# Kernel tuning notes

Measured on AMD Instinct MI355X. Metric: run time of the kernel, lower is better.

Reference implementation:

```python
import jax, jax.numpy as jnp
import numpy as np

T, D, E, F, K = 2048, 1024, 16, 512, 2  # tokens, hidden, experts, expert d_ff, top_k
NORM_TOPK = True


def setup_inputs() -> dict:
    key = jax.random.key(0)
    k0, k1, k2, k3 = jax.random.split(key, 4)
    hidden_states = jax.random.normal(k0, (T, D), jnp.float32)
    w_gate = jax.random.normal(k1, (E, D), jnp.float32) * (D ** -0.5)      # router Linear(D, E), no bias
    w13 = jax.random.normal(k2, (E, 2 * F, D), jnp.float32) * (D ** -0.5)  # fused gate+up proj per expert
    w2 = jax.random.normal(k3, (E, D, F), jnp.float32) * (F ** -0.5)       # down proj per expert
    return {"hidden_states": hidden_states, "w_gate": w_gate, "w13": w13, "w2": w2}


def reference(hidden_states, w_gate, w13, w2):
    # Router: softmax (fp32) -> top-k -> optional renorm
    logits = hidden_states @ w_gate.T                                   # [T, E]
    probs = jax.nn.softmax(logits.astype(jnp.float32), axis=-1)
    weights, selected = jax.lax.top_k(probs, K)                          # [T, K]
    if NORM_TOPK:
        weights = weights / jnp.sum(weights, axis=-1, keepdims=True)
    weights = weights.astype(hidden_states.dtype)

    # Sparse combine matrix: combine[t, e] = routing weight iff expert e selected for token t
    combine = jnp.zeros((T, E), hidden_states.dtype)
    combine = combine.at[jnp.arange(T)[:, None], selected].add(weights)

    # Expert FFN (computed for all experts, zeroed by combine; faithful math)
    h = jnp.einsum('td,efd->tef', hidden_states, w13)                    # [T, E, 2F]
    gate, up = jnp.split(h, 2, axis=-1)
    act = jax.nn.silu(gate) * up                                         # SiluAndMul, [T, E, F]
    y = jnp.einsum('tef,edf->ted', act, w2)                              # [T, E, D]
    return jnp.einsum('ted,te->td', y, combine)                          # [T, D]
```

## Files before the change

kernel.cpp:

```cpp
#include <hip/hip_runtime.h>
#include <hip/hip_bf16.h>
#include <math.h>

#define T_TOK 2048
#define DIM   1024
#define NEXP  16
#define FDIM  512
#define TOPK  2

#define BM 128
#define BN 64
#define BK 32

typedef float f32x4 __attribute__((ext_vector_type(4)));
typedef short s16x8 __attribute__((ext_vector_type(8)));

static __device__ __forceinline__ ushort f2bf(float f) {
  union { float f; unsigned u; } v; v.f = f;
  unsigned u = v.u;
  unsigned r = u + 0x7fffu + ((u >> 16) & 1u);
  return (ushort)(r >> 16);
}
static __device__ __forceinline__ float bf2f(ushort h) {
  union { unsigned u; float f; } v; v.u = ((unsigned)h) << 16; return v.f;
}
static __device__ __forceinline__ void split2(float f, ushort& h, ushort& l) {
  ushort hb = f2bf(f);
  h = hb;
  l = f2bf(f - bf2f(hb));
}

__global__ __launch_bounds__(64) void router_k(const float* __restrict__ x,
                                               const float* __restrict__ wg,
                                               int* __restrict__ sel,
                                               float* __restrict__ wt,
                                               int* __restrict__ cnt) {
  int t = blockIdx.x;
  int lane = threadIdx.x;
  const float* xr = x + (size_t)t * DIM;
  float acc[NEXP];
#pragma unroll
  for (int e = 0; e < NEXP; ++e) acc[e] = 0.f;
  for (int d0 = 0; d0 < DIM; d0 += 64) {
    float xv = xr[d0 + lane];
#pragma unroll
    for (int e = 0; e < NEXP; ++e) acc[e] += xv * wg[e * DIM + d0 + lane];
  }
#pragma unroll
  for (int e = 0; e < NEXP; ++e) {
    float v = acc[e];
    v += __shfl_xor(v, 32); v += __shfl_xor(v, 16); v += __shfl_xor(v, 8);
    v += __shfl_xor(v, 4);  v += __shfl_xor(v, 2);  v += __shfl_xor(v, 1);
    acc[e] = v;
  }
  if (lane == 0) {
    float b1 = -1e30f, b2 = -1e30f; int i1 = 0, i2 = 0;
#pragma unroll
    for (int e = 0; e < NEXP; ++e) {
      float v = acc[e];
      if (v > b1) { b2 = b1; i2 = i1; b1 = v; i1 = e; }
      else if (v > b2) { b2 = v; i2 = e; }
    }
    float r = expf(b2 - b1);
    float w2v = r / (1.f + r);
    float w1v = 1.f - w2v;
    sel[t * 2 + 0] = i1; sel[t * 2 + 1] = i2;
    wt[t * 2 + 0] = w1v; wt[t * 2 + 1] = w2v;
    atomicAdd(&cnt[i1], 1);
    atomicAdd(&cnt[i2], 1);
  }
}

__global__ __launch_bounds__(256) void xsplit_k(const float* __restrict__ x,
                                                ushort* __restrict__ xhi,
                                                ushort* __restrict__ xlo) {
  int idx = (blockIdx.x * 256 + threadIdx.x) * 4;
  float4 v = *(const float4*)(x + idx);
  ushort h0,h1,h2,h3,l0,l1,l2,l3;
  split2(v.x, h0, l0); split2(v.y, h1, l1);
  split2(v.z, h2, l2); split2(v.w, h3, l3);
  *(ushort4*)(xhi + idx) = make_ushort4(h0, h1, h2, h3);
  *(ushort4*)(xlo + idx) = make_ushort4(l0, l1, l2, l3);
}

__global__ void offsets_k(const int* __restrict__ cnt, int* __restrict__ off) {
  if (threadIdx.x == 0 && blockIdx.x == 0) {
    int s = 0;
#pragma unroll
    for (int e = 0; e < NEXP; ++e) { off[e] = s; s += cnt[e]; }
    off[NEXP] = s;
  }
}

__global__ __launch_bounds__(256) void fill_k(const int* __restrict__ sel,
                                              const float* __restrict__ wt,
                                              const int* __restrict__ off,
                                              int* __restrict__ cnt2,
                                              int* __restrict__ rowtok,
                                              float* __restrict__ rowwt) {
  int i = blockIdx.x * 256 + threadIdx.x;
  if (i >= T_TOK * TOPK) return;
  int e = sel[i];
  int pos = off[e] + atomicAdd(&cnt2[e], 1);
  rowtok[pos] = i >> 1;
  rowwt[pos] = wt[i];
}

__global__ __launch_bounds__(256, 2) void gemm1_k(const ushort* __restrict__ xhi,
                                                  const ushort* __restrict__ xlo,
                                                  const float* __restrict__ w13,
                                                  const int* __restrict__ off,
                                                  const int* __restrict__ rowtok,
                                                  float* __restrict__ H) {
  int e = blockIdx.z;
  int rbeg = off[e];
  int rows = off[e + 1] - rbeg;
  int m0 = blockIdx.y * BM;
  if (m0 >= rows) return;
  int n0 = blockIdx.x * BN;

  __shared__ ushort Ah[BM * BK], Al[BM * BK], Bh[BN * BK], Bl[BN * BK];
  __shared__ int toksh[BM];

  int tid = threadIdx.x;
  if (tid < BM) {
    int r = m0 + tid;
    toksh[tid] = rowtok[rbeg + (r < rows ? r : rows - 1)];
  }
  __syncthreads();

  int srow = tid >> 2;
  int sc = tid & 3;
  int tok0 = toksh[srow];
  int tok1 = toksh[srow + 64];
  const ushort* a0h = xhi + (size_t)tok0 * DIM + sc * 8;
  const ushort* a0l = xlo + (size_t)tok0 * DIM + sc * 8;
  const ushort* a1h = xhi + (size_t)tok1 * DIM + sc * 8;
  const ushort* a1l = xlo + (size_t)tok1 * DIM + sc * 8;
  const float*  bsrc = w13 + ((size_t)e * (2 * FDIM) + (n0 + srow)) * DIM + sc * 8;

  int boA0 = (srow * 64 + sc * 16) ^ ((srow & 7) << 4);
  int boA1 = ((srow + 64) * 64 + sc * 16) ^ ((srow & 7) << 4);
  int boB  = boA0;

  f32x4 acc[4][2];
#pragma unroll
  for (int a = 0; a < 4; ++a)
#pragma unroll
    for (int b = 0; b < 2; ++b) acc[a][b] = {0.f, 0.f, 0.f, 0.f};

  int lane = tid & 63;
  int w = tid >> 6;
  int wm = (w & 1) * 64, wn = (w >> 1) * 32;
  int lr = lane & 15, lk = lane >> 4;

  uint4 rA0h, rA0l, rA1h, rA1l;
  float4 rB0, rB1;

  rA0h = *(const uint4*)(a0h); rA0l = *(const uint4*)(a0l);
  rA1h = *(const uint4*)(a1h); rA1l = *(const uint4*)(a1l);
  rB0 = *(const float4*)(bsrc); rB1 = *(const float4*)(bsrc + 4);

  const int NS = DIM / BK;
  for (int ks = 0; ks < NS; ++ks) {
    __syncthreads();
    *(uint4*)((char*)Ah + boA0) = rA0h;
    *(uint4*)((char*)Al + boA0) = rA0l;
    *(uint4*)((char*)Ah + boA1) = rA1h;
    *(uint4*)((char*)Al + boA1) = rA1l;
    {
      float fv[8] = {rB0.x, rB0.y, rB0.z, rB0.w, rB1.x, rB1.y, rB1.z, rB1.w};
      uint hp[4], lp[4];
#pragma unroll
      for (int j = 0; j < 4; ++j) {
        ushort ha, la, hb, lb;
        split2(fv[2 * j], ha, la);
        split2(fv[2 * j + 1], hb, lb);
        hp[j] = (uint)ha | ((uint)hb << 16);
        lp[j] = (uint)la | ((uint)lb << 16);
      }
      *(uint4*)((char*)Bh + boB) = make_uint4(hp[0], hp[1], hp[2], hp[3]);
      *(uint4*)((char*)Bl + boB) = make_uint4(lp[0], lp[1], lp[2], lp[3]);
    }
    if (ks + 1 < NS) {
      int kb = (ks + 1) * BK;
      rA0h = *(const uint4*)(a0h + kb); rA0l = *(const uint4*)(a0l + kb);
      rA1h = *(const uint4*)(a1h + kb); rA1l = *(const uint4*)(a1l + kb);
      rB0 = *(const float4*)(bsrc + kb); rB1 = *(const float4*)(bsrc + kb + 4);
    }
    __syncthreads();

    s16x8 ah[4], al[4], bh[2], bl[2];
#pragma unroll
    for (int fm = 0; fm < 4; ++fm) {
      int row = wm + fm * 16 + lr;
      int bo = (row * 64 + lk * 16) ^ ((row & 7) << 4);
      ah[fm] = *(const s16x8*)((char*)Ah + bo);
      al[fm] = *(const s16x8*)((char*)Al + bo);
    }
#pragma unroll
    for (int fn = 0; fn < 2; ++fn) {
      int row = wn + fn * 16 + lr;
      int bo = (row * 64 + lk * 16) ^ ((row & 7) << 4);
      bh[fn] = *(const s16x8*)((char*)Bh + bo);
      bl[fn] = *(const s16x8*)((char*)Bl + bo);
    }
#pragma unroll
    for (int fm = 0; fm < 4; ++fm)
#pragma unroll
      for (int fn = 0; fn < 2; ++fn) {
        acc[fm][fn] = __builtin_amdgcn_mfma_f32_16x16x32_bf16(ah[fm], bh[fn], acc[fm][fn], 0, 0, 0);
        acc[fm][fn] = __builtin_amdgcn_mfma_f32_16x16x32_bf16(ah[fm], bl[fn], acc[fm][fn], 0, 0, 0);
        acc[fm][fn] = __builtin_amdgcn_mfma_f32_16x16x32_bf16(al[fm], bh[fn], acc[fm][fn], 0, 0, 0);
      }
  }

#pragma unroll
  for (int fm = 0; fm < 4; ++fm) {
    int rloc = wm + fm * 16 + lk * 4;
#pragma unroll
    for (int j = 0; j < 4; ++j) {
      int row = rloc + j;
      if (m0 + row < rows) {
        size_t gr = (size_t)(rbeg + m0 + row) * (2 * FDIM);
#pragma unroll
        for (int fn = 0; fn < 2; ++fn)
          H[gr + n0 + wn + fn * 16 + lr] = acc[fm][fn][j];
      }
    }
  }
}

__global__ __launch_bounds__(256) void act_k(const float* __restrict__ H,
                                             ushort* __restrict__ ahi,
                                             ushort* __restrict__ alo) {
  int idx = (blockIdx.x * 256 + threadIdx.x) * 4;
  int r = idx >> 9;
  int f = idx & 511;
  const float* hrow = H + (size_t)r * (2 * FDIM);
  float4 g = *(const float4*)(hrow + f);
  float4 u = *(const float4*)(hrow + FDIM + f);
  float a0 = g.x / (1.f + expf(-g.x)) * u.x;
  float a1 = g.y / (1.f + expf(-g.y)) * u.y;
  float a2 = g.z / (1.f + expf(-g.z)) * u.z;
  float a3 = g.w / (1.f + expf(-g.w)) * u.w;
  ushort h0,h1,h2,h3,l0,l1,l2,l3;
  split2(a0, h0, l0); split2(a1, h1, l1);
  split2(a2, h2, l2); split2(a3, h3, l3);
  *(ushort4*)(ahi + (size_t)r * FDIM + f) = make_ushort4(h0, h1, h2, h3);
  *(ushort4*)(alo + (size_t)r * FDIM + f) = make_ushort4(l0, l1, l2, l3);
}

__global__ __launch_bounds__(256, 2) void gemm2_k(const ushort* __restrict__ ahi,
                                                  const ushort* __restrict__ alo,
                                                  const float* __restrict__ w2,
                                                  const int* __restrict__ off,
                                                  const int* __restrict__ rowtok,
                                                  const float* __restrict__ rowwt,
                                                  float* __restrict__ out) {
  int e = blockIdx.z;
  int rbeg = off[e];
  int rows = off[e + 1] - rbeg;
  int m0 = blockIdx.y * BM;
  if (m0 >= rows) return;
  int n0 = blockIdx.x * BN;

  __shared__ ushort Ah[BM * BK], Al[BM * BK], Bh[BN * BK], Bl[BN * BK];
  __shared__ int toksh[BM];
  __shared__ float wtsh[BM];

  int tid = threadIdx.x;
  if (tid < BM) {
    int r = m0 + tid;
    int rr = rbeg + (r < rows ? r : rows - 1);
    toksh[tid] = rowtok[rr];
    wtsh[tid] = (r < rows) ? rowwt[rr] : 0.f;
  }
  __syncthreads();

  int srow = tid >> 2;
  int sc = tid & 3;
  int rg0 = m0 + srow;       rg0 = (rg0 < rows ? rg0 : rows - 1);
  int rg1 = m0 + srow + 64;  rg1 = (rg1 < rows ? rg1 : rows - 1);
  const ushort* a0h = ahi + (size_t)(rbeg + rg0) * FDIM + sc * 8;
  const ushort* a0l = alo + (size_t)(rbeg + rg0) * FDIM + sc * 8;
  const ushort* a1h = ahi + (size_t)(rbeg + rg1) * FDIM + sc * 8;
  const ushort* a1l = alo + (size_t)(rbeg + rg1) * FDIM + sc * 8;
  const float*  bsrc = w2 + ((size_t)e * DIM + (n0 + srow)) * FDIM + sc * 8;

  int boA0 = (srow * 64 + sc * 16) ^ ((srow & 7) << 4);
  int boA1 = ((srow + 64) * 64 + sc * 16) ^ ((srow & 7) << 4);
  int boB  = boA0;

  f32x4 acc[4][2];
#pragma unroll
  for (int a = 0; a < 4; ++a)
#pragma unroll
    for (int b = 0; b < 2; ++b) acc[a][b] = {0.f, 0.f, 0.f, 0.f};

  int lane = tid & 63;
  int w = tid >> 6;
  int wm = (w & 1) * 64, wn = (w >> 1) * 32;
  int lr = lane & 15, lk = lane >> 4;

  uint4 rA0h, rA0l, rA1h, rA1l;
  float4 rB0, rB1;
  rA0h = *(const uint4*)(a0h); rA0l = *(const uint4*)(a0l);
  rA1h = *(const uint4*)(a1h); rA1l = *(const uint4*)(a1l);
  rB0 = *(const float4*)(bsrc); rB1 = *(const float4*)(bsrc + 4);

  const int NS = FDIM / BK;
  for (int ks = 0; ks < NS; ++ks) {
    __syncthreads();
    *(uint4*)((char*)Ah + boA0) = rA0h;
    *(uint4*)((char*)Al + boA0) = rA0l;
    *(uint4*)((char*)Ah + boA1) = rA1h;
    *(uint4*)((char*)Al + boA1) = rA1l;
    {
      float fv[8] = {rB0.x, rB0.y, rB0.z, rB0.w, rB1.x, rB1.y, rB1.z, rB1.w};
      uint hp[4], lp[4];
#pragma unroll
      for (int j = 0; j < 4; ++j) {
        ushort ha, la, hb, lb;
        split2(fv[2 * j], ha, la);
        split2(fv[2 * j + 1], hb, lb);
        hp[j] = (uint)ha | ((uint)hb << 16);
        lp[j] = (uint)la | ((uint)lb << 16);
      }
      *(uint4*)((char*)Bh + boB) = make_uint4(hp[0], hp[1], hp[2], hp[3]);
      *(uint4*)((char*)Bl + boB) = make_uint4(lp[0], lp[1], lp[2], lp[3]);
    }
    if (ks + 1 < NS) {
      int kb = (ks + 1) * BK;
      rA0h = *(const uint4*)(a0h + kb); rA0l = *(const uint4*)(a0l + kb);
      rA1h = *(const uint4*)(a1h + kb); rA1l = *(const uint4*)(a1l + kb);
      rB0 = *(const float4*)(bsrc + kb); rB1 = *(const float4*)(bsrc + kb + 4);
    }
    __syncthreads();

    s16x8 ah[4], al[4], bh[2], bl[2];
#pragma unroll
    for (int fm = 0; fm < 4; ++fm) {
      int row = wm + fm * 16 + lr;
      int bo = (row * 64 + lk * 16) ^ ((row & 7) << 4);
      ah[fm] = *(const s16x8*)((char*)Ah + bo);
      al[fm] = *(const s16x8*)((char*)Al + bo);
    }
#pragma unroll
    for (int fn = 0; fn < 2; ++fn) {
      int row = wn + fn * 16 + lr;
      int bo = (row * 64 + lk * 16) ^ ((row & 7) << 4);
      bh[fn] = *(const s16x8*)((char*)Bh + bo);
      bl[fn] = *(const s16x8*)((char*)Bl + bo);
    }
#pragma unroll
    for (int fm = 0; fm < 4; ++fm)
#pragma unroll
      for (int fn = 0; fn < 2; ++fn) {
        acc[fm][fn] = __builtin_amdgcn_mfma_f32_16x16x32_bf16(ah[fm], bh[fn], acc[fm][fn], 0, 0, 0);
        acc[fm][fn] = __builtin_amdgcn_mfma_f32_16x16x32_bf16(ah[fm], bl[fn], acc[fm][fn], 0, 0, 0);
        acc[fm][fn] = __builtin_amdgcn_mfma_f32_16x16x32_bf16(al[fm], bh[fn], acc[fm][fn], 0, 0, 0);
      }
  }

#pragma unroll
  for (int fm = 0; fm < 4; ++fm) {
    int rloc = wm + fm * 16 + lk * 4;
#pragma unroll
    for (int j = 0; j < 4; ++j) {
      int row = rloc + j;
      if (m0 + row < rows) {
        int tok = toksh[row];
        float wgt = wtsh[row];
        float* orow = out + (size_t)tok * DIM + n0;
#pragma unroll
        for (int fn = 0; fn < 2; ++fn)
          atomicAdd(orow + wn + fn * 16 + lr, wgt * acc[fm][fn][j]);
      }
    }
  }
}

extern "C" void kernel_launch(void* const* d_in, const int* in_sizes, int n_in,
                              void* d_out, int out_size, void* d_ws, size_t ws_size,
                              hipStream_t stream) {
  const float* x   = (const float*)d_in[0];
  const float* wg  = (const float*)d_in[1];
  const float* w13 = (const float*)d_in[2];
  const float* w2  = (const float*)d_in[3];
  float* out = (float*)d_out;

  char* ws = (char*)d_ws;
  int*   cnt    = (int*)(ws + 0);
  int*   cnt2   = (int*)(ws + 64);
  int*   off    = (int*)(ws + 128);
  int*   sel    = (int*)(ws + 1024);
  float* wt     = (float*)(ws + 1024 + 16384);
  int*   rowtok = (int*)(ws + 1024 + 32768);
  float* rowwt  = (float*)(ws + 1024 + 49152);
  size_t o = 128 * 1024;
  ushort* xhi = (ushort*)(ws + o); o += (size_t)T_TOK * DIM * 2;
  ushort* xlo = (ushort*)(ws + o); o += (size_t)T_TOK * DIM * 2;
  float*  H   = (float*)(ws + o);  o += (size_t)T_TOK * TOPK * 2 * FDIM * 4;
  ushort* ahi = (ushort*)(ws + o); o += (size_t)T_TOK * TOPK * FDIM * 2;
  ushort* alo = (ushort*)(ws + o); o += (size_t)T_TOK * TOPK * FDIM * 2;

  hipMemsetAsync(ws, 0, 256, stream);
  hipMemsetAsync(d_out, 0, (size_t)out_size * sizeof(float), stream);

  router_k<<<T_TOK, 64, 0, stream>>>(x, wg, sel, wt, cnt);
  xsplit_k<<<(T_TOK * DIM) / 1024, 256, 0, stream>>>(x, xhi, xlo);
  offsets_k<<<1, 64, 0, stream>>>(cnt, off);
  fill_k<<<(T_TOK * TOPK + 255) / 256, 256, 0, stream>>>(sel, wt, off, cnt2, rowtok, rowwt);

  dim3 g1(2 * FDIM / BN, T_TOK / BM, NEXP);
  gemm1_k<<<g1, 256, 0, stream>>>(xhi, xlo, w13, off, rowtok, H);

  act_k<<<(T_TOK * TOPK * FDIM) / 1024, 256, 0, stream>>>(H, ahi, alo);

  dim3 g2(DIM / BN, T_TOK / BM, NEXP);
  gemm2_k<<<g2, 256, 0, stream>>>(ahi, alo, w2, off, rowtok, rowwt, out);
}
```

Baseline: 313.9 us.

## Deepen global prefetch to two stages and use raw barriers in MoE GEMMs

Both expert GEMM kernels now keep two register sets of prefetched global tiles, loading two K-steps ahead instead of one, with the loop manually unrolled by two. __syncthreads is replaced by an explicit lgkmcnt wait plus s_barrier and sched_barrier, so outstanding global loads are not forced to complete at each barrier. The aim is to hide global memory latency behind MFMA work. The cost is extra registers for the second prefetch set, which under launch_bounds(256,2) could cause spills, and the sched_barrier fences limit how the compiler can interleave instructions.

New measurement: 293.6 us. -6.5%, faster.

```diff
diff --git a/kernel.cpp b/kernel.cpp
--- a/kernel.cpp
+++ b/kernel.cpp
@@ -106,6 +106,66 @@
   rowwt[pos] = wt[i];
 }
 
+#define DECL_SET(S) uint4 pAh0##S, pAl0##S, pAh1##S, pAl1##S; float4 pB0##S, pB1##S;
+
+#define LOAD_SET(S, KB)                                                      \
+  pAh0##S = *(const uint4*)(a0h + (KB)); pAl0##S = *(const uint4*)(a0l + (KB)); \
+  pAh1##S = *(const uint4*)(a1h + (KB)); pAl1##S = *(const uint4*)(a1l + (KB)); \
+  pB0##S = *(const float4*)(bsrc + (KB)); pB1##S = *(const float4*)(bsrc + (KB) + 4);
+
+#define MOE_KSTEP(S, KS, NSv)                                                \
+  do {                                                                       \
+    asm volatile("s_waitcnt lgkmcnt(0)" ::: "memory");   \
+    __builtin_amdgcn_s_barrier();               \
+    __builtin_amdgcn_sched_barrier(0);                                       \
+    *(uint4*)((char*)Ah + boA0) = pAh0##S;                                   \
+    *(uint4*)((char*)Al + boA0) = pAl0##S;                                   \
+    *(uint4*)((char*)Ah + boA1) = pAh1##S;                                   \
+    *(uint4*)((char*)Al + boA1) = pAl1##S;                                   \
+    {                                                                        \
+      float fv[8] = {pB0##S.x, pB0##S.y, pB0##S.z, pB0##S.w,                 \
+                     pB1##S.x, pB1##S.y, pB1##S.z, pB1##S.w};                \
+      uint hp[4], lp[4];                                                     \
+      _Pragma("unroll")                                                      \
+      for (int j = 0; j < 4; ++j) {                                          \
+        ushort ha, la, hb, lb;                                               \
+        split2(fv[2 * j], ha, la);                                           \
+        split2(fv[2 * j + 1], hb, lb);                                       \
+        hp[j] = (uint)ha | ((uint)hb << 16);                                 \
+        lp[j] = (uint)la | ((uint)lb << 16);                                 \
+      }                                                                      \
+      *(uint4*)((char*)Bh + boB) = make_uint4(hp[0], hp[1], hp[2], hp[3]);   \
+      *(uint4*)((char*)Bl + boB) = make_uint4(lp[0], lp[1], lp[2], lp[3]);   \
+    }                                                                        \
+    if ((KS) + 2 < (NSv)) { int kb = ((KS) + 2) * BK; LOAD_SET(S, kb) }      \
+    asm volatile("s_waitcnt lgkmcnt(0)" ::: "memory");  \
+    __builtin_amdgcn_s_barrier();             \
+    __builtin_amdgcn_sched_barrier(0);                                       \
+    s16x8 ah[4], al[4], bh[2], bl[2];                                        \
+    _Pragma("unroll")                                                        \
+    for (int fm = 0; fm < 4; ++fm) {                                         \
+      int row = wm + fm * 16 + lr;                                           \
+      int bo = (row * 64 + lk * 16) ^ ((row & 7) << 4);                      \
+      ah[fm] = *(const s16x8*)((char*)Ah + bo);                              \
+      al[fm] = *(const s16x8*)((char*)Al + bo);                              \
+    }                                                                        \
+    _Pragma("unroll")                                                        \
+    for (int fn = 0; fn < 2; ++fn) {                                         \
+      int row = wn + fn * 16 + lr;                                           \
+      int bo = (row * 64 + lk * 16) ^ ((row & 7) << 4);                      \
+      bh[fn] = *(const s16x8*)((char*)Bh + bo);                              \
+      bl[fn] = *(const s16x8*)((char*)Bl + bo);                              \
+    }                                                                        \
+    _Pragma("unroll")                                                        \
+    for (int fm = 0; fm < 4; ++fm)                                           \
+      _Pragma("unroll")                                                      \
+      for (int fn = 0; fn < 2; ++fn) {                                       \
+        acc[fm][fn] = __builtin_amdgcn_mfma_f32_16x16x32_bf16(ah[fm], bh[fn], acc[fm][fn], 0, 0, 0); \
+        acc[fm][fn] = __builtin_amdgcn_mfma_f32_16x16x32_bf16(ah[fm], bl[fn], acc[fm][fn], 0, 0, 0); \
+        acc[fm][fn] = __builtin_amdgcn_mfma_f32_16x16x32_bf16(al[fm], bh[fn], acc[fm][fn], 0, 0, 0); \
+      }                                                                      \
+  } while (0)
+
 __global__ __launch_bounds__(256, 2) void gemm1_k(const ushort* __restrict__ xhi,
                                                   const ushort* __restrict__ xlo,
                                                   const float* __restrict__ w13,
@@ -154,65 +214,14 @@
   int wm = (w & 1) * 64, wn = (w >> 1) * 32;
   int lr = lane & 15, lk = lane >> 4;
 
-  uint4 rA0h, rA0l, rA1h, rA1l;
-  float4 rB0, rB1;
-
-  rA0h = *(const uint4*)(a0h); rA0l = *(const uint4*)(a0l);
-  rA1h = *(const uint4*)(a1h); rA1l = *(const uint4*)(a1l);
-  rB0 = *(const float4*)(bsrc); rB1 = *(const float4*)(bsrc + 4);
+  DECL_SET(_A) DECL_SET(_B)
+  LOAD_SET(_A, 0)
+  LOAD_SET(_B, BK)
 
   const int NS = DIM / BK;
-  for (int ks = 0; ks < NS; ++ks) {
-    __syncthreads();
-    *(uint4*)((char*)Ah + boA0) = rA0h;
-    *(uint4*)((char*)Al + boA0) = rA0l;
-    *(uint4*)((char*)Ah + boA1) = rA1h;
-    *(uint4*)((char*)Al + boA1) = rA1l;
-    {
-      float fv[8] = {rB0.x, rB0.y, rB0.z, rB0.w, rB1.x, rB1.y, rB1.z, rB1.w};
-      uint hp[4], lp[4];
-#pragma unroll
-      for (int j = 0; j < 4; ++j) {
-        ushort ha, la, hb, lb;
-        split2(fv[2 * j], ha, la);
-        split2(fv[2 * j + 1], hb, lb);
-        hp[j] = (uint)ha | ((uint)hb << 16);
-        lp[j] = (uint)la | ((uint)lb << 16);
-      }
-      *(uint4*)((char*)Bh + boB) = make_uint4(hp[0], hp[1], hp[2], hp[3]);
-      *(uint4*)((char*)Bl + boB) = make_uint4(lp[0], lp[1], lp[2], lp[3]);
-    }
-    if (ks + 1 < NS) {
-      int kb = (ks + 1) * BK;
-      rA0h = *(const uint4*)(a0h + kb); rA0l = *(const uint4*)(a0l + kb);
-      rA1h = *(const uint4*)(a1h + kb); rA1l = *(const uint4*)(a1l + kb);
-      rB0 = *(const float4*)(bsrc + kb); rB1 = *(const float4*)(bsrc + kb + 4);
-    }
-    __syncthreads();
-
-    s16x8 ah[4], al[4], bh[2], bl[2];
-#pragma unroll
-    for (int fm = 0; fm < 4; ++fm) {
-      int row = wm + fm * 16 + lr;
-      int bo = (row * 64 + lk * 16) ^ ((row & 7) << 4);
-      ah[fm] = *(const s16x8*)((char*)Ah + bo);
-      al[fm] = *(const s16x8*)((char*)Al + bo);
-    }
-#pragma unroll
-    for (int fn = 0; fn < 2; ++fn) {
-      int row = wn + fn * 16 + lr;
-      int bo = (row * 64 + lk * 16) ^ ((row & 7) << 4);
-      bh[fn] = *(const s16x8*)((char*)Bh + bo);
-      bl[fn] = *(const s16x8*)((char*)Bl + bo);
-    }
-#pragma unroll
-    for (int fm = 0; fm < 4; ++fm)
-#pragma unroll
-      for (int fn = 0; fn < 2; ++fn) {
-        acc[fm][fn] = __builtin_amdgcn_mfma_f32_16x16x32_bf16(ah[fm], bh[fn], acc[fm][fn], 0, 0, 0);
-        acc[fm][fn] = __builtin_amdgcn_mfma_f32_16x16x32_bf16(ah[fm], bl[fn], acc[fm][fn], 0, 0, 0);
-        acc[fm][fn] = __builtin_amdgcn_mfma_f32_16x16x32_bf16(al[fm], bh[fn], acc[fm][fn], 0, 0, 0);
-      }
+  for (int ks = 0; ks < NS; ks += 2) {
+    MOE_KSTEP(_A, ks, NS);
+    MOE_KSTEP(_B, ks + 1, NS);
   }
 
 #pragma unroll
@@ -303,64 +312,14 @@
   int wm = (w & 1) * 64, wn = (w >> 1) * 32;
   int lr = lane & 15, lk = lane >> 4;
 
-  uint4 rA0h, rA0l, rA1h, rA1l;
-  float4 rB0, rB1;
-  rA0h = *(const uint4*)(a0h); rA0l = *(const uint4*)(a0l);
-  rA1h = *(const uint4*)(a1h); rA1l = *(const uint4*)(a1l);
-  rB0 = *(const float4*)(bsrc); rB1 = *(const float4*)(bsrc + 4);
+  DECL_SET(_A) DECL_SET(_B)
+  LOAD_SET(_A, 0)
+  LOAD_SET(_B, BK)
 
   const int NS = FDIM / BK;
-  for (int ks = 0; ks < NS; ++ks) {
-    __syncthreads();
-    *(uint4*)((char*)Ah + boA0) = rA0h;
-    *(uint4*)((char*)Al + boA0) = rA0l;
-    *(uint4*)((char*)Ah + boA1) = rA1h;
-    *(uint4*)((char*)Al + boA1) = rA1l;
-    {
-      float fv[8] = {rB0.x, rB0.y, rB0.z, rB0.w, rB1.x, rB1.y, rB1.z, rB1.w};
-      uint hp[4], lp[4];
-#pragma unroll
-      for (int j = 0; j < 4; ++j) {
-        ushort ha, la, hb, lb;
-        split2(fv[2 * j], ha, la);
-        split2(fv[2 * j + 1], hb, lb);
-        hp[j] = (uint)ha | ((uint)hb << 16);
-        lp[j] = (uint)la | ((uint)lb << 16);
-      }
-      *(uint4*)((char*)Bh + boB) = make_uint4(hp[0], hp[1], hp[2], hp[3]);
-      *(uint4*)((char*)Bl + boB) = make_uint4(lp[0], lp[1], lp[2], lp[3]);
-    }
-    if (ks + 1 < NS) {
-      int kb = (ks + 1) * BK;
-      rA0h = *(const uint4*)(a0h + kb); rA0l = *(const uint4*)(a0l + kb);
-      rA1h = *(const uint4*)(a1h + kb); rA1l = *(const uint4*)(a1l + kb);
-      rB0 = *(const float4*)(bsrc + kb); rB1 = *(const float4*)(bsrc + kb + 4);
-    }
-    __syncthreads();
-
-    s16x8 ah[4], al[4], bh[2], bl[2];
-#pragma unroll
-    for (int fm = 0; fm < 4; ++fm) {
-      int row = wm + fm * 16 + lr;
-      int bo = (row * 64 + lk * 16) ^ ((row & 7) << 4);
-      ah[fm] = *(const s16x8*)((char*)Ah + bo);
-      al[fm] = *(const s16x8*)((char*)Al + bo);
-    }
-#pragma unroll
-    for (int fn = 0; fn < 2; ++fn) {
-      int row = wn + fn * 16 + lr;
-      int bo = (row * 64 + lk * 16) ^ ((row & 7) << 4);
-      bh[fn] = *(const s16x8*)((char*)Bh + bo);
-      bl[fn] = *(const s16x8*)((char*)Bl + bo);
-    }
-#pragma unroll
-    for (int fm = 0; fm < 4; ++fm)
-#pragma unroll
-      for (int fn = 0; fn < 2; ++fn) {
-        acc[fm][fn] = __builtin_amdgcn_mfma_f32_16x16x32_bf16(ah[fm], bh[fn], acc[fm][fn], 0, 0, 0);
-        acc[fm][fn] = __builtin_amdgcn_mfma_f32_16x16x32_bf16(ah[fm], bl[fn], acc[fm][fn], 0, 0, 0);
-        acc[fm][fn] = __builtin_amdgcn_mfma_f32_16x16x32_bf16(al[fm], bh[fn], acc[fm][fn], 0, 0, 0);
-      }
+  for (int ks = 0; ks < NS; ks += 2) {
+    MOE_KSTEP(_A, ks, NS);
+    MOE_KSTEP(_B, ks + 1, NS);
   }
 
 #pragma unroll
```
